# Kernel optimization log

Measured on AMD Instinct MI355X. Metric: run time of the kernel, lower is better.

The kernel has to match this reference:

```python
import jax, jax.numpy as jnp
import numpy as np

L, H, O, S, B = 128, 1024, 64, 256, 512  # latent, hidden, output, seq_len, batch
IN0 = L + O  # LSTM layer-0 input size


def setup_inputs() -> dict:
    key = jax.random.key(0)
    ks = jax.random.split(key, 16)
    sc = 0.05
    n = lambda k, shape: (jax.random.normal(k, shape, jnp.float32) * sc)
    return {
        "z": jax.random.normal(ks[0], (B, L), jnp.float32),
        "Wh": n(ks[1], (H, L)), "bh": jnp.zeros((H,), jnp.float32),
        "Wc": n(ks[2], (H, L)), "bc": jnp.zeros((H,), jnp.float32),
        "Wih0": n(ks[3], (4 * H, IN0)), "Whh0": n(ks[4], (4 * H, H)),
        "bih0": n(ks[5], (4 * H,)), "bhh0": n(ks[6], (4 * H,)),
        "Wih1": n(ks[7], (4 * H, H)), "Whh1": n(ks[8], (4 * H, H)),
        "bih1": n(ks[9], (4 * H,)), "bhh1": n(ks[10], (4 * H,)),
        "Wout": n(ks[11], (O, H)), "bout": jnp.zeros((O,), jnp.float32),
    }


def _lstm_cell(x, h, c, Wih, Whh, b):
    # PyTorch gate order: i, f, g, o
    gates = x @ Wih.T + h @ Whh.T + b  # (B, 4H)
    i, f, g, o = jnp.split(gates, 4, axis=-1)
    c_new = jax.nn.sigmoid(f) * c + jax.nn.sigmoid(i) * jnp.tanh(g)
    h_new = jax.nn.sigmoid(o) * jnp.tanh(c_new)
    return h_new, c_new


def reference(z, Wh, bh, Wc, bc, Wih0, Whh0, bih0, bhh0, Wih1, Whh1, bih1, bhh1, Wout, bout):
    batch = z.shape[0]
    # h_0 / c_0 are the same projection repeated for both layers
    h0 = z @ Wh.T + bh  # (B, H)
    c0 = z @ Wc.T + bc
    b0 = bih0 + bhh0
    b1 = bih1 + bhh1

    def step(carry, _):
        h1, c1, h2, c2, inp = carry
        x = jnp.concatenate([z, inp], axis=-1)  # (B, L+O)
        h1n, c1n = _lstm_cell(x, h1, c1, Wih0, Whh0, b0)
        h2n, c2n = _lstm_cell(h1n, h2, c2, Wih1, Whh1, b1)
        out = h2n @ Wout.T + bout  # (B, O) feeds back as next input
        return (h1n, c1n, h2n, c2n, out), out

    init = (h0, c0, h0, c0, jnp.zeros((batch, Wout.shape[0]), z.dtype))
    _, outs = jax.lax.scan(step, init, None, length=S)  # (S, B, O)
    return jnp.transpose(outs, (1, 0, 2))  # (B, S, O)
```

## Files before the change

### kernel.cpp

```cpp
#include <hip/hip_runtime.h>

#define Lz   128
#define Hd   1024
#define Od   64
#define Sq   256
#define Bt   512
#define K1   1216
#define K2q  2048
#define G4H  4096
#define NBLK 256u

typedef __attribute__((ext_vector_type(8))) short  short8;
typedef __attribute__((ext_vector_type(4))) float  floatx4;

__device__ __forceinline__ short f2bf(float x) {
  unsigned u = __float_as_uint(x);
  unsigned r = (u + 0x7fffu + ((u >> 16) & 1u)) >> 16;
  return (short)r;
}
__device__ __forceinline__ float sigf(float x)   { return 1.0f / (1.0f + __expf(-x)); }
__device__ __forceinline__ float tanhf_(float x) { return 1.0f - 2.0f / (__expf(2.0f * x) + 1.0f); }

__device__ __forceinline__ void gl_lds_z(const short* g, void* l) {
  __builtin_amdgcn_global_load_lds(
      (__attribute__((address_space(1))) const void*)g,
      (__attribute__((address_space(3))) void*)l, 16, 0, 0);
}
__device__ __forceinline__ void gl_lds_a(const short* g, void* l) {
  __builtin_amdgcn_global_load_lds(
      (__attribute__((address_space(1))) const void*)g,
      (__attribute__((address_space(3))) void*)l, 16, 0, 1);
}
__device__ __forceinline__ void gl_lds_w(const short* g, void* l) {
  __builtin_amdgcn_global_load_lds(
      (__attribute__((address_space(1))) const void*)g,
      (__attribute__((address_space(3))) void*)l, 16, 0, 2);
}
__device__ __forceinline__ void st_wt(short* p, short v) {
  asm volatile("global_store_short %0, %1, off sc0"
               :: "v"(p), "v"((unsigned)(unsigned short)v) : "memory");
}

#define S_BARRIER() asm volatile("s_barrier" ::: "memory")
#define WAITVM(n)   asm volatile("s_waitcnt vmcnt(" #n ")" ::: "memory")

__device__ __forceinline__ void xbar(int* b) {
  __syncthreads();
  if (threadIdx.x == 0) {
    unsigned* cnt = (unsigned*)b;
    unsigned* gen = (unsigned*)b + 1;
    unsigned g = __hip_atomic_load(gen, __ATOMIC_RELAXED, __HIP_MEMORY_SCOPE_AGENT);
    unsigned a = __hip_atomic_fetch_add(cnt, 1u, __ATOMIC_RELAXED, __HIP_MEMORY_SCOPE_AGENT);
    if (a == 31u) {
      __hip_atomic_store(cnt, 0u, __ATOMIC_RELAXED, __HIP_MEMORY_SCOPE_AGENT);
      __hip_atomic_store(gen, g + 1u, __ATOMIC_RELAXED, __HIP_MEMORY_SCOPE_AGENT);
    } else {
      while (__hip_atomic_load(gen, __ATOMIC_RELAXED, __HIP_MEMORY_SCOPE_AGENT) == g)
        __builtin_amdgcn_s_sleep(8);
    }
  }
  __syncthreads();
}

__device__ __forceinline__ int oldrow(int nr) {
  int bn = nr >> 6, rem = nr & 63, g = rem >> 4, jj = rem & 15;
  return g * Hd + bn * 16 + jj;
}

struct Params {
  const short *W1r, *W2r, *Woutb;
  const float *b0v, *b1v, *bout;
  short *A1_0, *A1_1, *A2_0, *A2_1;
  float *c1, *c2, *out;
  int *barr;
};

__global__ void k_conv_w1a(const float* __restrict__ Whh0, short* __restrict__ W1r) {
  int idx = blockIdx.x * 256 + threadIdx.x;
  int nr = idx >> 10, k = idx & 1023;
  W1r[nr * K1 + k] = f2bf(Whh0[oldrow(nr) * Hd + k]);
}
__global__ void k_conv_w1c(const float* __restrict__ Wih0, short* __restrict__ W1r) {
  int idx = blockIdx.x * 256 + threadIdx.x;
  int nr = idx >> 7, kz = idx & 127;
  W1r[nr * K1 + 1024 + kz] = f2bf(Wih0[oldrow(nr) * (Lz + Od) + kz]);
}
__global__ void k_conv_w1d(const float* __restrict__ Wih0, short* __restrict__ W1r) {
  int idx = blockIdx.x * 256 + threadIdx.x;
  int nr = idx >> 6, j = idx & 63;
  W1r[nr * K1 + 1152 + j] = f2bf(Wih0[oldrow(nr) * (Lz + Od) + Lz + j]);
}
__global__ void k_conv_w2(const float* __restrict__ Wih1, const float* __restrict__ Whh1,
                          short* __restrict__ W2r) {
  int idx = blockIdx.x * 256 + threadIdx.x;
  int nr = idx >> 11, k = idx & 2047;
  int orow = oldrow(nr);
  float v = (k < Hd) ? Wih1[orow * Hd + k] : Whh1[orow * Hd + (k - Hd)];
  W2r[nr * K2q + k] = f2bf(v);
}
__global__ void k_conv_wout(const float* __restrict__ Wout, short* __restrict__ Woutb) {
  int idx = blockIdx.x * 256 + threadIdx.x;
  Woutb[idx] = f2bf(Wout[idx]);
}
__global__ void k_vec(const float* __restrict__ bih0, const float* __restrict__ bhh0,
                      const float* __restrict__ bih1, const float* __restrict__ bhh1,
                      float* __restrict__ b0v, float* __restrict__ b1v,
                      int* __restrict__ barzero) {
  int n = blockIdx.x * 256 + threadIdx.x;
  if (n < 256) barzero[n] = 0;
  b0v[n] = bih0[n] + bhh0[n];
  b1v[n] = bih1[n] + bhh1[n];
}
__global__ void k_init(const float* __restrict__ z, const float* __restrict__ Wh,
                       const float* __restrict__ bh, const float* __restrict__ Wc,
                       const float* __restrict__ bc,
                       short* __restrict__ A1_0, short* __restrict__ A2_0,
                       float* __restrict__ c1, float* __restrict__ c2) {
  int idx = blockIdx.x * 256 + threadIdx.x;
  int m = idx >> 10, n = idx & 1023;
  const float* zr = z + m * Lz;
  const float* whr = Wh + n * Lz;
  const float* wcr = Wc + n * Lz;
  float hh = bh[n], cc = bc[n];
  #pragma unroll 8
  for (int k = 0; k < Lz; ++k) { float zv = zr[k]; hh += zv * whr[k]; cc += zv * wcr[k]; }
  c1[idx] = cc;
  c2[idx] = cc;
  short hb = f2bf(hh);
  A1_0[m * K1 + n] = hb;
  if (n < Od) A1_0[m * K1 + 1152 + n] = 0;
  A2_0[m * K2q + Hd + n] = hb;
}
__global__ void k_initz(const float* __restrict__ z, short* __restrict__ A1_0,
                        short* __restrict__ A1_1) {
  int idx = blockIdx.x * 256 + threadIdx.x;
  int m = idx >> 7, k = idx & 127;
  short v = f2bf(z[idx]);
  A1_0[m * K1 + 1024 + k] = v;
  A1_1[m * K1 + 1024 + k] = v;
}

#define MFMA16(a, b, c) __builtin_amdgcn_mfma_f32_16x16x32_bf16(a, b, c, 0, 0, 0)
#define BUFSH 12288
#define NBUF  4
#define LDS_BYTES (NBUF * BUFSH * 2)

__device__ __forceinline__ void out_reg(const short* __restrict__ h2src,
    const short* __restrict__ Wo, const float* __restrict__ boutv,
    float* __restrict__ outp, int tt, int mo,
    short* __restrict__ ofb, int tid, int* __restrict__ ocnt)
{
  const int lane = tid & 63, w = tid >> 6;
  const int l15 = lane & 15, q = lane >> 4;
  const short* ap = h2src + (size_t)(mo + l15) * K2q + Hd + q * 8;
  const short* bp = Wo + (size_t)(w * 16 + l15) * Hd + q * 8;
  floatx4 acc = {};
  short8 A0, B0, A1, B1, A2, B2, A3, B3;
#define OLA(r, kk) asm volatile("global_load_dwordx4 %0, %1, off sc0" \
    : "=v"(r) : "v"(ap + (kk) * 32) : "memory")
#define OLB(r, kk) asm volatile("global_load_dwordx4 %0, %1, off" \
    : "=v"(r) : "v"(bp + (kk) * 32) : "memory")
  OLA(A0, 0); OLB(B0, 0); OLA(A1, 1); OLB(B1, 1);
  OLA(A2, 2); OLB(B2, 2); OLA(A3, 3); OLB(B3, 3);
  #pragma unroll
  for (int g = 0; g < 16; g += 2) {
    WAITVM(4); __builtin_amdgcn_sched_barrier(0);
    acc = MFMA16(A0, B0, acc); acc = MFMA16(A1, B1, acc);
    if (g + 2 < 16) { OLA(A0, 2*(g+2)); OLB(B0, 2*(g+2));
                      OLA(A1, 2*(g+2)+1); OLB(B1, 2*(g+2)+1); }
    if (g + 3 < 16) { WAITVM(4); } else { WAITVM(0); }
    __builtin_amdgcn_sched_barrier(0);
    acc = MFMA16(A2, B2, acc); acc = MFMA16(A3, B3, acc);
    if (g + 3 < 16) { OLA(A2, 2*(g+3)); OLB(B2, 2*(g+3));
                      OLA(A3, 2*(g+3)+1); OLB(B3, 2*(g+3)+1); }
  }
#undef OLA
#undef OLB
  #pragma unroll
  for (int r = 0; r < 4; ++r) {
    int m = mo + q * 4 + r;
    int n = w * 16 + l15;
    float v = acc[r] + boutv[n];
    outp[(size_t)m * (Sq * Od) + (size_t)tt * Od + n] = v;
    if (ofb) st_wt(ofb + (size_t)m * K1 + 1152 + n, f2bf(v));
  }
  WAITVM(0);
  __syncthreads();
  if (ocnt && tid == 0)
    __hip_atomic_fetch_add(ocnt, 1, __ATOMIC_RELAXED, __HIP_MEMORY_SCOPE_AGENT);
}

__device__ __forceinline__ void gemm_win(
    const short* __restrict__ Asrc, int astride, int nk, int zstart,
    const short* __restrict__ Wsrc,
    const float* __restrict__ bz, float cr[2][4],
    short* __restrict__ hd0, int hs0, int ho0,
    short* __restrict__ hd1, int hs1, int ho1,
    int m0, int bn2, short* sm, int tid,
    int* __restrict__ ocnt, int othresh)
{
  const int lane = tid & 63, w = tid >> 6;
  const int l15 = lane & 15, q = lane >> 4;
  const int mh = w >> 1, gh = w & 1;
  floatx4 acc[2][4] = {};

  const short* Ab = Asrc + (size_t)m0 * astride;
  const short* Wb = Wsrc + (size_t)(bn2 * 128) * astride;

  auto stage = [&](int kk, int b) {
    const int kb = kk * 64;
    short* as = sm + b * BUFSH;
    short* ws = as + 4096;
    const bool stat = (kk == zstart) || (kk == zstart + 1);
    #pragma unroll
    for (int i = 0; i < 2; ++i) {
      int s = i * 256 + tid;
      int row = s >> 3, cg = (s & 7) ^ (row & 7);
      const short* gp = Ab + (size_t)row * astride + kb + cg * 8;
      if (stat) gl_lds_z(gp, as + s * 8);
      else      gl_lds_a(gp, as + s * 8);
    }
    #pragma unroll
    for (int i = 0; i < 4; ++i) {
      int s = i * 256 + tid;
      int row = s >> 3, cg = (s & 7) ^ (row & 7);
      gl_lds_w(Wb + (size_t)row * astride + kb + cg * 8, ws + s * 8);
    }
  };

  stage(0, 0);
  stage(1, 1);
  stage(2, 2);
  for (int kk = 0; kk < nk; ++kk) {
    S_BARRIER();
    if (kk + 3 < nk) {
      if (ocnt && kk + 3 == nk - 1) {
        while (__hip_atomic_load(ocnt, __ATOMIC_RELAXED, __HIP_MEMORY_SCOPE_AGENT) < othresh)
          __builtin_amdgcn_s_sleep(1);
      }
      stage(kk + 3, (kk + 3) & 3);
      WAITVM(18);
    }
    else if (kk + 2 < nk) { WAITVM(12); }
    else if (kk + 1 < nk) { WAITVM(6); }
    else { WAITVM(0); }
    S_BARRIER();
    const short* as = sm + (kk & 3) * BUFSH;
    const short* ws = as + 4096;
    #pragma unroll
    for (int ks = 0; ks < 2; ++ks) {
      const int cc = ks * 4 + q;
      short8 a[2];
      #pragma unroll
      for (int mt = 0; mt < 2; ++mt) {
        const int ra = mh * 32 + mt * 16 + l15;
        a[mt] = *(const short8*)(as + (ra * 8 + (cc ^ (ra & 7))) * 8);
      }
      #pragma unroll
      for (int g = 0; g < 4; ++g) {
        const int rw = gh * 64 + g * 16 + l15;
        short8 b = *(const short8*)(ws + (rw * 8 + (cc ^ (rw & 7))) * 8);
        acc[0][g] = MFMA16(a[0], b, acc[0][g]);
        acc[1][g] = MFMA16(a[1], b, acc[1][g]);
      }
    }
  }
  #pragma unroll
  for (int mt = 0; mt < 2; ++mt) {
    #pragma unroll
    for (int r = 0; r < 4; ++r) {
      const int mg = m0 + mh * 32 + mt * 16 + q * 4 + r;
      const int colh = bn2 * 32 + gh * 16 + l15;
      float iv = acc[mt][0][r] + bz[0];
      float fv = acc[mt][1][r] + bz[1];
      float gv = acc[mt][2][r] + bz[2];
      float ov = acc[mt][3][r] + bz[3];
      float cn = sigf(fv) * cr[mt][r] + sigf(iv) * tanhf_(gv);
      cr[mt][r] = cn;
      short hb = f2bf(sigf(ov) * tanhf_(cn));
      st_wt(hd0 + (size_t)mg * hs0 + ho0 + colh, hb);
      if (hd1) st_wt(hd1 + (size_t)mg * hs1 + ho1 + colh, hb);
    }
  }
}

__global__ __launch_bounds__(256, 1) void lstm_main(Params p) {
  extern __shared__ __align__(16) short smem[];
  const int tid = threadIdx.x;

  __shared__ int sh_ids[2];
  if (tid == 0) {
    unsigned xr;
    asm volatile("s_getreg_b32 %0, hwreg(HW_REG_XCC_ID)" : "=s"(xr));
    int xcc = (int)(xr & 7u);
    int slot = (int)__hip_atomic_fetch_add((unsigned*)(p.barr + xcc * 16 + 3), 1u,
                                           __ATOMIC_RELAXED, __HIP_MEMORY_SCOPE_AGENT);
    sh_ids[0] = xcc;
    sh_ids[1] = slot & 31;
  }
  __syncthreads();
  const int xcc  = sh_ids[0];
  const int slot = sh_ids[1];
  int* xb = p.barr + xcc * 16;

  const int m0 = xcc * 64;
  const int bn2 = slot;
  const bool ojob = ((slot & 7) == 0);
  const int mo = xcc * 64 + (slot >> 3) * 16;

  const int lane = tid & 63, w = tid >> 6;
  const int l15 = lane & 15, q = lane >> 4;
  const int mh = w >> 1, gh = w & 1;
  const int colh = bn2 * 32 + gh * 16 + l15;

  float bA[4], bB[4], c1r[2][4], c2r[2][4];
  #pragma unroll
  for (int g = 0; g < 4; ++g) {
    bA[g] = p.b0v[g * Hd + colh];
    bB[g] = p.b1v[g * Hd + colh];
  }
  #pragma unroll
  for (int mt = 0; mt < 2; ++mt)
    #pragma unroll
    for (int r = 0; r < 4; ++r) {
      const int mg = m0 + mh * 32 + mt * 16 + q * 4 + r;
      c1r[mt][r] = p.c1[mg * Hd + colh];
      c2r[mt][r] = p.c2[mg * Hd + colh];
    }

  for (int t = 0; t < Sq; ++t) {
    const int par = t & 1;
    const short* A1p = par ? p.A1_1 : p.A1_0;
    short* A1n = par ? p.A1_0 : p.A1_1;
    short* A2p = par ? p.A2_1 : p.A2_0;
    short* A2n = par ? p.A2_0 : p.A2_1;
    if (ojob && t > 0)
      out_reg(A2p, p.Woutb, p.bout, p.out, t - 1, mo, (short*)A1p, tid, xb + 2);
    gemm_win(A1p, K1, 19, 16, p.W1r, bA, c1r,
             A1n, K1, 0, (short*)A2p, K2q, 0, m0, bn2, smem, tid,
             xb + 2, 4 * t);
    xbar(xb);
    gemm_win(A2p, K2q, 32, -2, p.W2r, bB, c2r,
             A2n, K2q, Hd, (short*)nullptr, 0, 0, m0, bn2, smem, tid,
             nullptr, 0);
    xbar(xb);
  }
  if (ojob)
    out_reg(p.A2_0, p.Woutb, p.bout, p.out, Sq - 1, mo, (short*)nullptr, tid, nullptr);
}

extern "C" void kernel_launch(void* const* d_in, const int* in_sizes, int n_in,
                              void* d_out, int out_size, void* d_ws, size_t ws_size,
                              hipStream_t stream) {
  const float* z    = (const float*)d_in[0];
  const float* Wh   = (const float*)d_in[1];
  const float* bh   = (const float*)d_in[2];
  const float* Wc   = (const float*)d_in[3];
  const float* bc   = (const float*)d_in[4];
  const float* Wih0 = (const float*)d_in[5];
  const float* Whh0 = (const float*)d_in[6];
  const float* bih0 = (const float*)d_in[7];
  const float* bhh0 = (const float*)d_in[8];
  const float* Wih1 = (const float*)d_in[9];
  const float* Whh1 = (const float*)d_in[10];
  const float* bih1 = (const float*)d_in[11];
  const float* bhh1 = (const float*)d_in[12];
  const float* Wout = (const float*)d_in[13];
  const float* bout = (const float*)d_in[14];
  float* out = (float*)d_out;

  char* ws = (char*)d_ws;
  size_t off = 0;
  auto carve = [&](size_t bytes) { char* p = ws + off; off = (off + bytes + 255) & ~size_t(255); return p; };
  short* W1r   = (short*)carve((size_t)G4H * K1 * 2);
  short* W2r   = (short*)carve((size_t)G4H * K2q * 2);
  short* Woutb = (short*)carve((size_t)Od * Hd * 2);
  float* b0v   = (float*)carve(G4H * 4);
  float* b1v   = (float*)carve(G4H * 4);
  short* A1_0  = (short*)carve((size_t)Bt * K1 * 2);
  short* A1_1  = (short*)carve((size_t)Bt * K1 * 2);
  short* A2_0  = (short*)carve((size_t)Bt * K2q * 2);
  short* A2_1  = (short*)carve((size_t)Bt * K2q * 2);
  float* c1    = (float*)carve((size_t)Bt * Hd * 4);
  float* c2    = (float*)carve((size_t)Bt * Hd * 4);
  int*   barr  = (int*)carve(1024);

  k_conv_w1a<<<16384, 256, 0, stream>>>(Whh0, W1r);
  k_conv_w1c<<<2048, 256, 0, stream>>>(Wih0, W1r);
  k_conv_w1d<<<1024, 256, 0, stream>>>(Wih0, W1r);
  k_conv_w2 <<<32768, 256, 0, stream>>>(Wih1, Whh1, W2r);
  k_conv_wout<<<256, 256, 0, stream>>>(Wout, Woutb);
  k_vec<<<16, 256, 0, stream>>>(bih0, bhh0, bih1, bhh1, b0v, b1v, barr);
  k_init<<<2048, 256, 0, stream>>>(z, Wh, bh, Wc, bc, A1_0, A2_0, c1, c2);
  k_initz<<<256, 256, 0, stream>>>(z, A1_0, A1_1);

  Params pr{W1r, W2r, Woutb, b0v, b1v, bout,
            A1_0, A1_1, A2_0, A2_1, c1, c2, out, barr};

  (void)hipFuncSetAttribute((const void*)lstm_main,
                            hipFuncAttributeMaxDynamicSharedMemorySize, LDS_BYTES);
  lstm_main<<<dim3(NBLK), dim3(256), LDS_BYTES, stream>>>(pr);
}
```

Baseline: 12.29 ms.

## Pair XCDs per 128-row batch slab with XCC-local activation copies and exchange

The work split changes from one 64-row batch tile per XCD (each XCD sweeping all 4H gate columns) to one 128-row slab per pair of XCDs, with each XCD computing half of the hidden columns. Each XCD keeps its own copy of the activation buffers, written with XCC-local stores. Hidden states are also published to global exchange buffers (sc0 sc1), and the partner half is copied into the local copy after a pair-wide barrier. The aim is to let each XCD stream only half the weights, keeping them L2-resident, and to hit local L2 for activations. The cost is extra exchange copies and barrier phases per timestep, plus cache-policy changes on the loads.

```diff
diff --git a/kernel.cpp b/kernel.cpp
--- a/kernel.cpp
+++ b/kernel.cpp
@@ -9,6 +9,8 @@
 #define K2q  2048
 #define G4H  4096
 #define NBLK 256u
+#define A1LS (128*1024)
+#define A2LS (128*2048)
 
 typedef __attribute__((ext_vector_type(8))) short  short8;
 typedef __attribute__((ext_vector_type(4))) float  floatx4;
@@ -21,7 +23,7 @@
 __device__ __forceinline__ float sigf(float x)   { return 1.0f / (1.0f + __expf(-x)); }
 __device__ __forceinline__ float tanhf_(float x) { return 1.0f - 2.0f / (__expf(2.0f * x) + 1.0f); }
 
-__device__ __forceinline__ void gl_lds_z(const short* g, void* l) {
+__device__ __forceinline__ void gl_lds_c(const short* g, void* l) {
   __builtin_amdgcn_global_load_lds(
       (__attribute__((address_space(1))) const void*)g,
       (__attribute__((address_space(3))) void*)l, 16, 0, 0);
@@ -31,13 +33,17 @@
       (__attribute__((address_space(1))) const void*)g,
       (__attribute__((address_space(3))) void*)l, 16, 0, 1);
 }
-__device__ __forceinline__ void gl_lds_w(const short* g, void* l) {
+__device__ __forceinline__ void gl_lds_f(const short* g, void* l) {
   __builtin_amdgcn_global_load_lds(
       (__attribute__((address_space(1))) const void*)g,
-      (__attribute__((address_space(3))) void*)l, 16, 0, 2);
-}
-__device__ __forceinline__ void st_wt(short* p, short v) {
+      (__attribute__((address_space(3))) void*)l, 16, 0, 19);
+}
+__device__ __forceinline__ void st_l(short* p, short v) {
   asm volatile("global_store_short %0, %1, off sc0"
+               :: "v"(p), "v"((unsigned)(unsigned short)v) : "memory");
+}
+__device__ __forceinline__ void st_g(short* p, short v) {
+  asm volatile("global_store_short %0, %1, off sc0 sc1"
                :: "v"(p), "v"((unsigned)(unsigned short)v) : "memory");
 }
 
@@ -51,7 +57,7 @@
     unsigned* gen = (unsigned*)b + 1;
     unsigned g = __hip_atomic_load(gen, __ATOMIC_RELAXED, __HIP_MEMORY_SCOPE_AGENT);
     unsigned a = __hip_atomic_fetch_add(cnt, 1u, __ATOMIC_RELAXED, __HIP_MEMORY_SCOPE_AGENT);
-    if (a == 31u) {
+    if (a == 63u) {
       __hip_atomic_store(cnt, 0u, __ATOMIC_RELAXED, __HIP_MEMORY_SCOPE_AGENT);
       __hip_atomic_store(gen, g + 1u, __ATOMIC_RELAXED, __HIP_MEMORY_SCOPE_AGENT);
     } else {
@@ -70,7 +76,8 @@
 struct Params {
   const short *W1r, *W2r, *Woutb;
   const float *b0v, *b1v, *bout;
-  short *A1_0, *A1_1, *A2_0, *A2_1;
+  short *A1L, *A2L;
+  short *E1, *E2, *Eout, *Zb;
   float *c1, *c2, *out;
   int *barr;
 };
@@ -105,16 +112,18 @@
 __global__ void k_vec(const float* __restrict__ bih0, const float* __restrict__ bhh0,
                       const float* __restrict__ bih1, const float* __restrict__ bhh1,
                       float* __restrict__ b0v, float* __restrict__ b1v,
-                      int* __restrict__ barzero) {
+                      int* __restrict__ barzero, int* __restrict__ eoutz) {
   int n = blockIdx.x * 256 + threadIdx.x;
   if (n < 256) barzero[n] = 0;
+  #pragma unroll
+  for (int j = 0; j < 4; ++j) eoutz[n * 4 + j] = 0;
   b0v[n] = bih0[n] + bhh0[n];
   b1v[n] = bih1[n] + bhh1[n];
 }
 __global__ void k_init(const float* __restrict__ z, const float* __restrict__ Wh,
                        const float* __restrict__ bh, const float* __restrict__ Wc,
                        const float* __restrict__ bc,
-                       short* __restrict__ A1_0, short* __restrict__ A2_0,
+                       short* __restrict__ A1L, short* __restrict__ A2L,
                        float* __restrict__ c1, float* __restrict__ c2) {
   int idx = blockIdx.x * 256 + threadIdx.x;
   int m = idx >> 10, n = idx & 1023;
@@ -127,17 +136,15 @@
   c1[idx] = cc;
   c2[idx] = cc;
   short hb = f2bf(hh);
-  A1_0[m * K1 + n] = hb;
-  if (n < Od) A1_0[m * K1 + 1152 + n] = 0;
-  A2_0[m * K2q + Hd + n] = hb;
-}
-__global__ void k_initz(const float* __restrict__ z, short* __restrict__ A1_0,
-                        short* __restrict__ A1_1) {
-  int idx = blockIdx.x * 256 + threadIdx.x;
-  int m = idx >> 7, k = idx & 127;
-  short v = f2bf(z[idx]);
-  A1_0[m * K1 + 1024 + k] = v;
-  A1_1[m * K1 + 1024 + k] = v;
+  int x0 = (m >> 7) * 2, lr = m & 127;
+  short* a1 = A1L + ((size_t)0 * 8 + x0) * A1LS + (size_t)lr * 1024 + n;
+  a1[0] = hb; a1[A1LS] = hb;
+  short* a2 = A2L + ((size_t)x0) * A2LS + (size_t)lr * 2048 + 1024 + n;
+  a2[0] = hb; a2[A2LS] = hb;
+}
+__global__ void k_zb(const float* __restrict__ z, short* __restrict__ Zb) {
+  int idx = blockIdx.x * 256 + threadIdx.x;
+  Zb[idx] = f2bf(z[idx]);
 }
 
 #define MFMA16(a, b, c) __builtin_amdgcn_mfma_f32_16x16x32_bf16(a, b, c, 0, 0, 0)
@@ -145,14 +152,34 @@
 #define NBUF  4
 #define LDS_BYTES (NBUF * BUFSH * 2)
 
-__device__ __forceinline__ void out_reg(const short* __restrict__ h2src,
+__device__ __forceinline__ void xchg(const short* __restrict__ Esrc,
+    short* __restrict__ d0, int s0, int o0,
+    short* __restrict__ d1, int xhalf, int slot, int tid)
+{
+  const int row = slot * 4 + (tid >> 6);
+  const int col = ((xhalf ^ 1) << 9) + (tid & 63) * 8;
+  const short* src = Esrc + (size_t)row * 1024 + col;
+  short8 v;
+  asm volatile("global_load_dwordx4 %0, %1, off sc0 sc1 nt"
+               : "=v"(v) : "v"(src) : "memory");
+  WAITVM(0);
+  short* p0 = d0 + (size_t)row * s0 + o0 + col;
+  asm volatile("global_store_dwordx4 %0, %1, off sc0" :: "v"(p0), "v"(v) : "memory");
+  if (d1) {
+    short* p1 = d1 + (size_t)row * 1024 + col;
+    asm volatile("global_store_dwordx4 %0, %1, off sc0" :: "v"(p1), "v"(v) : "memory");
+  }
+  WAITVM(0);
+}
+
+__device__ __forceinline__ void out_reg(const short* __restrict__ A2c,
     const short* __restrict__ Wo, const float* __restrict__ boutv,
-    float* __restrict__ outp, int tt, int mo,
-    short* __restrict__ ofb, int tid, int* __restrict__ ocnt)
+    float* __restrict__ outp, int tt, int mo, int pid,
+    short* __restrict__ eout, int tid, int* __restrict__ ocnt)
 {
   const int lane = tid & 63, w = tid >> 6;
   const int l15 = lane & 15, q = lane >> 4;
-  const short* ap = h2src + (size_t)(mo + l15) * K2q + Hd + q * 8;
+  const short* ap = A2c + (size_t)(mo + l15) * 2048 + 1024 + q * 8;
   const short* bp = Wo + (size_t)(w * 16 + l15) * Hd + q * 8;
   floatx4 acc = {};
   short8 A0, B0, A1, B1, A2, B2, A3, B3;
@@ -181,8 +208,8 @@
     int m = mo + q * 4 + r;
     int n = w * 16 + l15;
     float v = acc[r] + boutv[n];
-    outp[(size_t)m * (Sq * Od) + (size_t)tt * Od + n] = v;
-    if (ofb) st_wt(ofb + (size_t)m * K1 + 1152 + n, f2bf(v));
+    outp[(size_t)(pid * 128 + m) * (Sq * Od) + (size_t)tt * Od + n] = v;
+    if (eout) st_g(eout + (size_t)m * 64 + n, f2bf(v));
   }
   WAITVM(0);
   __syncthreads();
@@ -190,41 +217,49 @@
     __hip_atomic_fetch_add(ocnt, 1, __ATOMIC_RELAXED, __HIP_MEMORY_SCOPE_AGENT);
 }
 
+template<int MODE>
 __device__ __forceinline__ void gemm_win(
-    const short* __restrict__ Asrc, int astride, int nk, int zstart,
+    const short* __restrict__ pA,
+    const short* __restrict__ pZ,
+    const short* __restrict__ pEo,
     const short* __restrict__ Wsrc,
     const float* __restrict__ bz, float cr[2][4],
     short* __restrict__ hd0, int hs0, int ho0,
-    short* __restrict__ hd1, int hs1, int ho1,
-    int m0, int bn2, short* sm, int tid,
+    short* __restrict__ hd1, int hs1,
+    short* __restrict__ hg,
+    int mrow0, int bn2, short* sm, int tid,
     int* __restrict__ ocnt, int othresh)
 {
+  const int nk = MODE ? 19 : 32;
+  const int wstr = MODE ? K1 : K2q;
+  const int astr = MODE ? 1024 : 2048;
   const int lane = tid & 63, w = tid >> 6;
   const int l15 = lane & 15, q = lane >> 4;
   const int mh = w >> 1, gh = w & 1;
   floatx4 acc[2][4] = {};
 
-  const short* Ab = Asrc + (size_t)m0 * astride;
-  const short* Wb = Wsrc + (size_t)(bn2 * 128) * astride;
+  const short* Wb = Wsrc + (size_t)(bn2 * 128) * wstr;
 
   auto stage = [&](int kk, int b) {
-    const int kb = kk * 64;
     short* as = sm + b * BUFSH;
     short* ws = as + 4096;
-    const bool stat = (kk == zstart) || (kk == zstart + 1);
     #pragma unroll
     for (int i = 0; i < 2; ++i) {
       int s = i * 256 + tid;
       int row = s >> 3, cg = (s & 7) ^ (row & 7);
-      const short* gp = Ab + (size_t)row * astride + kb + cg * 8;
-      if (stat) gl_lds_z(gp, as + s * 8);
-      else      gl_lds_a(gp, as + s * 8);
+      if (MODE == 1) {
+        if (kk < 16)      gl_lds_a(pA + (size_t)row * astr + kk * 64 + cg * 8, as + s * 8);
+        else if (kk < 18) gl_lds_c(pZ + (size_t)row * 128 + (kk - 16) * 64 + cg * 8, as + s * 8);
+        else              gl_lds_f(pEo + (size_t)row * 64 + cg * 8, as + s * 8);
+      } else {
+        gl_lds_a(pA + (size_t)row * astr + kk * 64 + cg * 8, as + s * 8);
+      }
     }
     #pragma unroll
     for (int i = 0; i < 4; ++i) {
       int s = i * 256 + tid;
       int row = s >> 3, cg = (s & 7) ^ (row & 7);
-      gl_lds_w(Wb + (size_t)row * astride + kb + cg * 8, ws + s * 8);
+      gl_lds_c(Wb + (size_t)row * wstr + kk * 64 + cg * 8, ws + s * 8);
     }
   };
 
@@ -234,7 +269,7 @@
   for (int kk = 0; kk < nk; ++kk) {
     S_BARRIER();
     if (kk + 3 < nk) {
-      if (ocnt && kk + 3 == nk - 1) {
+      if (MODE == 1 && ocnt && kk + 3 == nk - 1) {
         while (__hip_atomic_load(ocnt, __ATOMIC_RELAXED, __HIP_MEMORY_SCOPE_AGENT) < othresh)
           __builtin_amdgcn_s_sleep(1);
       }
@@ -265,12 +300,12 @@
       }
     }
   }
+  const int colh = bn2 * 32 + gh * 16 + l15;
   #pragma unroll
   for (int mt = 0; mt < 2; ++mt) {
     #pragma unroll
     for (int r = 0; r < 4; ++r) {
-      const int mg = m0 + mh * 32 + mt * 16 + q * 4 + r;
-      const int colh = bn2 * 32 + gh * 16 + l15;
+      const int mg = mrow0 + mh * 32 + mt * 16 + q * 4 + r;
       float iv = acc[mt][0][r] + bz[0];
       float fv = acc[mt][1][r] + bz[1];
       float gv = acc[mt][2][r] + bz[2];
@@ -278,8 +313,9 @@
       float cn = sigf(fv) * cr[mt][r] + sigf(iv) * tanhf_(gv);
       cr[mt][r] = cn;
       short hb = f2bf(sigf(ov) * tanhf_(cn));
-      st_wt(hd0 + (size_t)mg * hs0 + ho0 + colh, hb);
-      if (hd1) st_wt(hd1 + (size_t)mg * hs1 + ho1 + colh, hb);
+      st_l(hd0 + (size_t)mg * hs0 + ho0 + colh, hb);
+      if (MODE == 1) st_l(hd1 + (size_t)mg * hs1 + colh, hb);
+      st_g(hg + (size_t)mg * 1024 + colh, hb);
     }
   }
 }
@@ -293,26 +329,35 @@
     unsigned xr;
     asm volatile("s_getreg_b32 %0, hwreg(HW_REG_XCC_ID)" : "=s"(xr));
     int xcc = (int)(xr & 7u);
-    int slot = (int)__hip_atomic_fetch_add((unsigned*)(p.barr + xcc * 16 + 3), 1u,
+    int slot = (int)__hip_atomic_fetch_add((unsigned*)(p.barr + 128 + xcc), 1u,
                                            __ATOMIC_RELAXED, __HIP_MEMORY_SCOPE_AGENT);
     sh_ids[0] = xcc;
     sh_ids[1] = slot & 31;
   }
   __syncthreads();
-  const int xcc  = sh_ids[0];
-  const int slot = sh_ids[1];
-  int* xb = p.barr + xcc * 16;
-
-  const int m0 = xcc * 64;
-  const int bn2 = slot;
+  const int xcc   = sh_ids[0];
+  const int slot  = sh_ids[1];
+  const int pid   = xcc >> 1;
+  const int xhalf = xcc & 1;
+  int* pb = p.barr + pid * 16;
+
+  const int bn2 = xhalf * 16 + (slot & 15);
+  const int mrow0 = (slot >> 4) * 64;
   const bool ojob = ((slot & 7) == 0);
-  const int mo = xcc * 64 + (slot >> 3) * 16;
+  const int mo = (xhalf * 4 + (slot >> 3)) * 16;
+  const int grow = pid * 128;
 
   const int lane = tid & 63, w = tid >> 6;
   const int l15 = lane & 15, q = lane >> 4;
   const int mh = w >> 1, gh = w & 1;
   const int colh = bn2 * 32 + gh * 16 + l15;
 
+  short* E1p = p.E1 + (size_t)grow * 1024;
+  short* E2p = p.E2 + (size_t)grow * 1024;
+  short* Eoutp = p.Eout + (size_t)grow * 64;
+  const short* Zp  = p.Zb + (size_t)(grow + mrow0) * 128;
+  const short* Eop = p.Eout + (size_t)(grow + mrow0) * 64;
+
   float bA[4], bB[4], c1r[2][4], c2r[2][4];
   #pragma unroll
   for (int g = 0; g < 4; ++g) {
@@ -323,30 +368,44 @@
   for (int mt = 0; mt < 2; ++mt)
     #pragma unroll
     for (int r = 0; r < 4; ++r) {
-      const int mg = m0 + mh * 32 + mt * 16 + q * 4 + r;
+      const int mg = grow + mrow0 + mh * 32 + mt * 16 + q * 4 + r;
       c1r[mt][r] = p.c1[mg * Hd + colh];
       c2r[mt][r] = p.c2[mg * Hd + colh];
     }
 
   for (int t = 0; t < Sq; ++t) {
     const int par = t & 1;
-    const short* A1p = par ? p.A1_1 : p.A1_0;
-    short* A1n = par ? p.A1_0 : p.A1_1;
-    short* A2p = par ? p.A2_1 : p.A2_0;
-    short* A2n = par ? p.A2_0 : p.A2_1;
-    if (ojob && t > 0)
-      out_reg(A2p, p.Woutb, p.bout, p.out, t - 1, mo, (short*)A1p, tid, xb + 2);
-    gemm_win(A1p, K1, 19, 16, p.W1r, bA, c1r,
-             A1n, K1, 0, (short*)A2p, K2q, 0, m0, bn2, smem, tid,
-             xb + 2, 4 * t);
-    xbar(xb);
-    gemm_win(A2p, K2q, 32, -2, p.W2r, bB, c2r,
-             A2n, K2q, Hd, (short*)nullptr, 0, 0, m0, bn2, smem, tid,
-             nullptr, 0);
-    xbar(xb);
-  }
-  if (ojob)
-    out_reg(p.A2_0, p.Woutb, p.bout, p.out, Sq - 1, mo, (short*)nullptr, tid, nullptr);
+    short* A1c = p.A1L + ((size_t)par * 8 + xcc) * A1LS;
+    short* A1n = p.A1L + ((size_t)(par ^ 1) * 8 + xcc) * A1LS;
+    short* A2c = p.A2L + ((size_t)par * 8 + xcc) * A2LS;
+    short* A2n = p.A2L + ((size_t)(par ^ 1) * 8 + xcc) * A2LS;
+
+    if (t > 0) {
+      xchg(E2p, A2c, 2048, 1024, (short*)nullptr, xhalf, slot, tid);
+      xbar(pb);
+      if (ojob)
+        out_reg(A2c, p.Woutb, p.bout, p.out, t - 1, mo, pid, Eoutp, tid, pb + 2);
+    }
+    gemm_win<1>(A1c + (size_t)mrow0 * 1024, Zp, Eop, p.W1r, bA, c1r,
+                A1n, 1024, 0, A2c, 2048, E1p,
+                mrow0, bn2, smem, tid, pb + 2, 8 * t);
+    xbar(pb);
+    xchg(E1p, A2c, 2048, 0, A1n, xhalf, slot, tid);
+    xbar(pb);
+    gemm_win<0>(A2c + (size_t)mrow0 * 2048, (const short*)nullptr, (const short*)nullptr,
+                p.W2r, bB, c2r,
+                A2n, 2048, 1024, (short*)nullptr, 0, E2p,
+                mrow0, bn2, smem, tid, nullptr, 0);
+    xbar(pb);
+  }
+  {
+    short* A2f = p.A2L + (size_t)xcc * A2LS;
+    xchg(E2p, A2f, 2048, 1024, (short*)nullptr, xhalf, slot, tid);
+    xbar(pb);
+    if (ojob)
+      out_reg(A2f, p.Woutb, p.bout, p.out, Sq - 1, mo, pid,
+              (short*)nullptr, tid, nullptr);
+  }
 }
 
 extern "C" void kernel_launch(void* const* d_in, const int* in_sizes, int n_in,
@@ -377,10 +436,12 @@
   short* Woutb = (short*)carve((size_t)Od * Hd * 2);
   float* b0v   = (float*)carve(G4H * 4);
   float* b1v   = (float*)carve(G4H * 4);
-  short* A1_0  = (short*)carve((size_t)Bt * K1 * 2);
-  short* A1_1  = (short*)carve((size_t)Bt * K1 * 2);
-  short* A2_0  = (short*)carve((size_t)Bt * K2q * 2);
-  short* A2_1  = (short*)carve((size_t)Bt * K2q * 2);
+  short* A1L   = (short*)carve((size_t)2 * 8 * A1LS * 2);
+  short* A2L   = (short*)carve((size_t)2 * 8 * A2LS * 2);
+  short* E1    = (short*)carve((size_t)Bt * 1024 * 2);
+  short* E2    = (short*)carve((size_t)Bt * 1024 * 2);
+  short* Eout  = (short*)carve((size_t)Bt * Od * 2);
+  short* Zb    = (short*)carve((size_t)Bt * Lz * 2);
   float* c1    = (float*)carve((size_t)Bt * Hd * 4);
   float* c2    = (float*)carve((size_t)Bt * Hd * 4);
   int*   barr  = (int*)carve(1024);
@@ -390,12 +451,12 @@
   k_conv_w1d<<<1024, 256, 0, stream>>>(Wih0, W1r);
   k_conv_w2 <<<32768, 256, 0, stream>>>(Wih1, Whh1, W2r);
   k_conv_wout<<<256, 256, 0, stream>>>(Wout, Woutb);
-  k_vec<<<16, 256, 0, stream>>>(bih0, bhh0, bih1, bhh1, b0v, b1v, barr);
-  k_init<<<2048, 256, 0, stream>>>(z, Wh, bh, Wc, bc, A1_0, A2_0, c1, c2);
-  k_initz<<<256, 256, 0, stream>>>(z, A1_0, A1_1);
+  k_vec<<<16, 256, 0, stream>>>(bih0, bhh0, bih1, bhh1, b0v, b1v, barr, (int*)Eout);
+  k_init<<<2048, 256, 0, stream>>>(z, Wh, bh, Wc, bc, A1L, A2L, c1, c2);
+  k_zb<<<256, 256, 0, stream>>>(z, Zb);
 
   Params pr{W1r, W2r, Woutb, b0v, b1v, bout,
-            A1_0, A1_1, A2_0, A2_1, c1, c2, out, barr};
+            A1L, A2L, E1, E2, Eout, Zb, c1, c2, out, barr};
 
   (void)hipFuncSetAttribute((const void*)lstm_main,
                             hipFuncAttributeMaxDynamicSharedMemorySize, LDS_BYTES);
```

After: 13.82 ms. 1.12x slower.
